# Kernel optimization log

Hardware: AMD Instinct MI355X
Metric: run time of the kernel (lower is better)

The kernel has to match this reference:

```python
import jax, jax.numpy as jnp
import numpy as np

BN_EPS = 1e-5

def _conv1x1(x, w, b):
    # x: [B,C,H,W], w: [O,C], b: [O] -> [B,O,H,W]
    return jnp.einsum('bchw,oc->bohw', x, w) + b[None, :, None, None]

def _maxpool2(x):
    B, C, H, W = x.shape
    return x.reshape(B, C, H // 2, 2, W // 2, 2).max(axis=(3, 5))

def setup_inputs() -> dict:
    key = jax.random.key(0)
    ks = jax.random.split(key, 5)
    B, C, Cint, H, W = 8, 512, 256, 64, 64
    s = 1.0 / np.sqrt(C)
    s2 = 1.0 / np.sqrt(Cint)
    return {
        'x': jax.random.normal(ks[0], (B, C, H, W), jnp.float32),
        'g_w': jax.random.normal(ks[1], (Cint, C), jnp.float32) * s,
        'g_b': jnp.zeros((Cint,), jnp.float32),
        'theta_w': jax.random.normal(ks[2], (Cint, C), jnp.float32) * s,
        'theta_b': jnp.zeros((Cint,), jnp.float32),
        'phi_w': jax.random.normal(ks[3], (Cint, C), jnp.float32) * s,
        'phi_b': jnp.zeros((Cint,), jnp.float32),
        'w_w': jax.random.normal(ks[4], (C, Cint), jnp.float32) * s2,
        'w_b': jnp.zeros((C,), jnp.float32),
        'bn_gamma': jnp.ones((C,), jnp.float32),
        'bn_beta': jnp.zeros((C,), jnp.float32),
        'bn_mean': jnp.zeros((C,), jnp.float32),
        'bn_var': jnp.ones((C,), jnp.float32),
    }

def reference(x, g_w, g_b, theta_w, theta_b, phi_w, phi_b, w_w, w_b,
              bn_gamma, bn_beta, bn_mean, bn_var):
    B, C, H, W = x.shape
    Cint = g_w.shape[0]
    # projections (1x1 convs); g and phi are sub-sampled by MaxPool2d(2)
    xg = _maxpool2(_conv1x1(x, g_w, g_b)).reshape(B, Cint, -1)      # [B,Cint,M]
    xphi = _maxpool2(_conv1x1(x, phi_w, phi_b)).reshape(B, Cint, -1)  # [B,Cint,M]
    xth = _conv1x1(x, theta_w, theta_b).reshape(B, Cint, -1)        # [B,Cint,N]
    # affinity: theta^T @ phi -> [B,N,M], softmax over M
    f = jax.nn.softmax(jnp.einsum('bcn,bcm->bnm', xth, xphi), axis=-1)
    # weighted sum: f @ g^T -> [B,N,Cint] -> [B,Cint,H,W]
    y = jnp.einsum('bnm,bcm->bcn', f, xg).reshape(B, Cint, H, W)
    # output conv + batchnorm (inference form) + residual
    z = _conv1x1(y, w_w, w_b)
    inv = jax.lax.rsqrt(bn_var + BN_EPS)
    z = (z - bn_mean[None, :, None, None]) * (bn_gamma * inv)[None, :, None, None] + bn_beta[None, :, None, None]
    return z + x
```

## Files before the change

kernel.cpp:

```cpp
#include <hip/hip_runtime.h>
#include <cmath>


#define B_  8
#define C_  512
#define CI_ 256
#define N_  4096
#define M_  1024

typedef _Float16 half8 __attribute__((ext_vector_type(8)));
typedef _Float16 half4 __attribute__((ext_vector_type(4)));
typedef float    f32x4 __attribute__((ext_vector_type(4)));

__global__ __launch_bounds__(256) void wconv_kernel(
    const float* __restrict__ g_w, const float* __restrict__ th_w,
    const float* __restrict__ ph_w, const float* __restrict__ w_w,
    _Float16* __restrict__ wAll, _Float16* __restrict__ w16)
{
    const int i = blockIdx.x * 256 + threadIdx.x;
    if (i < 768 * 512) {
        const int o = i >> 9, c = i & 511;
        const float v = (o < 256) ? g_w[o * 512 + c]
                      : (o < 512) ? th_w[(o - 256) * 512 + c]
                                  : ph_w[(o - 512) * 512 + c];
        wAll[i] = (_Float16)v;
    } else {
        const int j = i - 768 * 512;
        w16[j] = (_Float16)w_w[j];
    }
}

__global__ __launch_bounds__(256) void xt_kernel(
    const float* __restrict__ x, _Float16* __restrict__ xT)
{
    __shared__ float Ls[64][68];
    const int t = threadIdx.x;
    const int n0 = blockIdx.x * 64, c0 = blockIdx.y * 64, b = blockIdx.z;

    const int row = t >> 4, coln = (t & 15) * 4;
    #pragma unroll
    for (int p = 0; p < 4; ++p) {
        const int c = p * 16 + row;
        *(float4*)&Ls[c][coln] = *(const float4*)&x[((size_t)b * C_ + c0 + c) * N_ + n0 + coln];
    }
    __syncthreads();
    const int nr = t >> 2, cq = (t & 3) * 16;
    _Float16 hv[16];
    #pragma unroll
    for (int j = 0; j < 16; ++j) hv[j] = (_Float16)Ls[cq + j][nr];
    _Float16* dst = &xT[((size_t)b * N_ + n0 + nr) * C_ + c0 + cq];
    *(half8*)&dst[0] = *(half8*)&hv[0];
    *(half8*)&dst[8] = *(half8*)&hv[8];
}

__global__ __launch_bounds__(256) void proj_kernel(
    const _Float16* __restrict__ xT, const _Float16* __restrict__ wAll,
    const float* __restrict__ g_b, const float* __restrict__ th_b,
    const float* __restrict__ ph_b,
    _Float16* __restrict__ thT, _Float16* __restrict__ phT, _Float16* __restrict__ g16)
{
    __shared__ __align__(16) char smem[27648];
    _Float16 (*Ws)[72] = (_Float16(*)[72])smem;
    _Float16 (*Xs)[72] = (_Float16(*)[72])(smem + 9216);
    _Float16 (*Yt)[72] = (_Float16(*)[72])smem;
    _Float16 (*Pp)[72] = (_Float16(*)[72])smem;
    _Float16 (*Pg)[40] = (_Float16(*)[40])smem;

    const int t = threadIdx.x;
    const int w = t >> 6, l = t & 63, l15 = l & 15, lg = l >> 4;
    const int bx = blockIdx.x, rt = blockIdx.y, b = blockIdx.z;
    const int r0 = rt * 64, n0 = bx * 128;

    f32x4 acc[8];
    #pragma unroll
    for (int f = 0; f < 8; ++f) acc[f] = (f32x4){0.f, 0.f, 0.f, 0.f};

    const int warow = t >> 2, wakq = (t & 3) * 16;
    const int xrow = t >> 1,  xkq = (t & 1) * 32;

    #pragma unroll 1
    for (int k0 = 0; k0 < C_; k0 += 64) {
        __syncthreads();
        {
            const _Float16* src = &wAll[(size_t)(r0 + warow) * C_ + k0 + wakq];
            *(half8*)&Ws[warow][wakq]     = *(const half8*)&src[0];
            *(half8*)&Ws[warow][wakq + 8] = *(const half8*)&src[8];
            const _Float16* xs = &xT[((size_t)b * N_ + n0 + xrow) * C_ + k0 + xkq];
            *(half8*)&Xs[xrow][xkq]      = *(const half8*)&xs[0];
            *(half8*)&Xs[xrow][xkq + 8]  = *(const half8*)&xs[8];
            *(half8*)&Xs[xrow][xkq + 16] = *(const half8*)&xs[16];
            *(half8*)&Xs[xrow][xkq + 24] = *(const half8*)&xs[24];
        }
        __syncthreads();
        #pragma unroll
        for (int ks = 0; ks < 2; ++ks) {
            half8 a = *(half8*)&Ws[w * 16 + l15][ks * 32 + lg * 8];
            #pragma unroll
            for (int f = 0; f < 8; ++f) {
                half8 bb = *(half8*)&Xs[f * 16 + l15][ks * 32 + lg * 8];
                acc[f] = __builtin_amdgcn_mfma_f32_16x16x32_f16(a, bb, acc[f], 0, 0, 0);
            }
        }
    }

    {
        const float* Bp = (rt < 4) ? g_b : (rt < 8) ? th_b : ph_b;
        const int coff = (rt < 4) ? 0 : (rt < 8) ? 256 : 512;
        float bias[4];
        #pragma unroll
        for (int r = 0; r < 4; ++r) bias[r] = Bp[r0 - coff + w * 16 + lg * 4 + r];
        #pragma unroll
        for (int f = 0; f < 8; ++f)
            #pragma unroll
            for (int r = 0; r < 4; ++r) acc[f][r] += bias[r];
    }

    if (rt >= 4 && rt < 8) {
        const int c0 = r0 - 256;
        __syncthreads();
        #pragma unroll
        for (int f = 0; f < 8; ++f) {
            half4 hv = { (_Float16)acc[f][0], (_Float16)acc[f][1],
                         (_Float16)acc[f][2], (_Float16)acc[f][3] };
            *(half4*)&Yt[f * 16 + l15][w * 16 + lg * 4] = hv;
        }
        __syncthreads();
        const int nr = t >> 1, oq = (t & 1) * 32;
        _Float16* dst = &thT[((size_t)b * N_ + n0 + nr) * CI_ + c0 + oq];
        #pragma unroll
        for (int j = 0; j < 4; ++j)
            *(half8*)&dst[j * 8] = *(half8*)&Yt[nr][oq + j * 8];
    } else {
        float pool[4][4];
        #pragma unroll
        for (int f = 0; f < 4; ++f)
            #pragma unroll
            for (int r = 0; r < 4; ++r) {
                const float v0 = acc[f][r], v1 = acc[f + 4][r];
                const float h0 = fmaxf(v0, __shfl_xor(v0, 1));
                const float h1 = fmaxf(v1, __shfl_xor(v1, 1));
                pool[f][r] = fmaxf(h0, h1);
            }
        __syncthreads();
        const bool isphi = (rt >= 8);
        const int c0 = isphi ? r0 - 512 : r0;
        if ((l15 & 1) == 0) {
            const int Wl = l15 >> 1;
            if (isphi) {
                #pragma unroll
                for (int f = 0; f < 4; ++f) {
                    half4 hv = { (_Float16)pool[f][0], (_Float16)pool[f][1],
                                 (_Float16)pool[f][2], (_Float16)pool[f][3] };
                    *(half4*)&Pp[f * 8 + Wl][w * 16 + lg * 4] = hv;
                }
            } else {
                #pragma unroll
                for (int f = 0; f < 4; ++f)
                    #pragma unroll
                    for (int r = 0; r < 4; ++r)
                        Pg[w * 16 + lg * 4 + r][f * 8 + Wl] = (_Float16)pool[f][r];
            }
        }
        __syncthreads();
        if (isphi) {
            const int row = t >> 3, cqq = (t & 7) * 8;
            *(half8*)&phT[((size_t)b * M_ + bx * 32 + row) * CI_ + c0 + cqq] =
                *(half8*)&Pp[row][cqq];
        } else {
            const int row = t >> 2, mq = (t & 3) * 8;
            *(half8*)&g16[((size_t)b * CI_ + r0 + row) * M_ + bx * 32 + mq] =
                *(half8*)&Pg[row][mq];
        }
    }
}

__global__ __launch_bounds__(256) void attn_kernel(
    const _Float16* __restrict__ thT, const _Float16* __restrict__ phT,
    const _Float16* __restrict__ g16, _Float16* __restrict__ y16)
{
    __shared__ __align__(16) char smem[61440];
    _Float16 (*Tl)[264] = (_Float16(*)[264])smem;
    _Float16 (*Ph)[72]  = (_Float16(*)[72])(smem + 33792);
    _Float16 (*Gl)[72]  = (_Float16(*)[72])(smem + 43008);
    _Float16 (*Pl)[72]  = (_Float16(*)[72])(smem + 52224);
    float    (*Yb)[69]  = (float(*)[69])(smem + 33792);

    const int t = threadIdx.x;
    const int w = t >> 6, l = t & 63;
    const int l15 = l & 15, lg = l >> 4;
    const int n0 = blockIdx.x * 64;
    const int b  = blockIdx.y;

    {
        const int row = t >> 2, cq = (t & 3) * 64;
        const _Float16* src = &thT[((size_t)b * N_ + n0 + row) * CI_ + cq];
        #pragma unroll
        for (int i = 0; i < 8; ++i)
            *(half8*)&Tl[row][cq + 8 * i] = *(const half8*)&src[8 * i];
    }

    f32x4 yacc[16];
    #pragma unroll
    for (int i = 0; i < 16; ++i) yacc[i] = (f32x4){0.f, 0.f, 0.f, 0.f};
    float m_run[4] = {-INFINITY, -INFINITY, -INFINITY, -INFINITY};
    float l_run[4] = {0.f, 0.f, 0.f, 0.f};

    const int srow = t >> 2, ssq = (t & 3) * 16;

    #pragma unroll 1
    for (int mt = 0; mt < 16; ++mt) {
        const int m0 = mt * 64;
        f32x4 sf[4];
        #pragma unroll
        for (int i = 0; i < 4; ++i) sf[i] = (f32x4){0.f, 0.f, 0.f, 0.f};

        #pragma unroll 1
        for (int cch = 0; cch < 4; ++cch) {
            __syncthreads();
            const _Float16* src = &phT[((size_t)b * M_ + m0 + srow) * CI_ + cch * 64 + ssq];
            *(half8*)&Ph[srow][ssq]     = *(const half8*)&src[0];
            *(half8*)&Ph[srow][ssq + 8] = *(const half8*)&src[8];
            __syncthreads();
            #pragma unroll
            for (int ks = 0; ks < 2; ++ks) {
                half8 a = *(half8*)&Tl[w * 16 + l15][cch * 64 + ks * 32 + lg * 8];
                #pragma unroll
                for (int mf = 0; mf < 4; ++mf) {
                    half8 bb = *(half8*)&Ph[mf * 16 + l15][ks * 32 + lg * 8];
                    sf[mf] = __builtin_amdgcn_mfma_f32_16x16x32_f16(a, bb, sf[mf], 0, 0, 0);
                }
            }
        }

        float sc[4];
        #pragma unroll
        for (int r = 0; r < 4; ++r) {
            float mx = fmaxf(fmaxf(sf[0][r], sf[1][r]), fmaxf(sf[2][r], sf[3][r]));
            #pragma unroll
            for (int off = 1; off < 16; off <<= 1) mx = fmaxf(mx, __shfl_xor(mx, off, 64));
            const float mnew = fmaxf(m_run[r], mx);
            sc[r] = __expf(m_run[r] - mnew);
            float sum = 0.f;
            #pragma unroll
            for (int mf = 0; mf < 4; ++mf) {
                const float p = __expf(sf[mf][r] - mnew);
                Pl[w * 16 + lg * 4 + r][mf * 16 + l15] = (_Float16)p;
                sum += p;
            }
            #pragma unroll
            for (int off = 1; off < 16; off <<= 1) sum += __shfl_xor(sum, off, 64);
            l_run[r] = l_run[r] * sc[r] + sum;
            m_run[r] = mnew;
        }
        #pragma unroll
        for (int i = 0; i < 16; ++i) {
            yacc[i][0] *= sc[0]; yacc[i][1] *= sc[1];
            yacc[i][2] *= sc[2]; yacc[i][3] *= sc[3];
        }

        #pragma unroll
        for (int cc = 0; cc < 4; ++cc) {
            __syncthreads();
            const _Float16* gs = &g16[((size_t)b * CI_ + cc * 64 + srow) * M_ + m0 + ssq];
            *(half8*)&Gl[srow][ssq]     = *(const half8*)&gs[0];
            *(half8*)&Gl[srow][ssq + 8] = *(const half8*)&gs[8];
            __syncthreads();
            half8 pa0 = *(half8*)&Pl[w * 16 + l15][lg * 8];
            half8 pa1 = *(half8*)&Pl[w * 16 + l15][32 + lg * 8];
            #pragma unroll
            for (int cf = 0; cf < 4; ++cf) {
                half8 b0 = *(half8*)&Gl[cf * 16 + l15][lg * 8];
                half8 b1 = *(half8*)&Gl[cf * 16 + l15][32 + lg * 8];
                yacc[cc * 4 + cf] = __builtin_amdgcn_mfma_f32_16x16x32_f16(pa0, b0, yacc[cc * 4 + cf], 0, 0, 0);
                yacc[cc * 4 + cf] = __builtin_amdgcn_mfma_f32_16x16x32_f16(pa1, b1, yacc[cc * 4 + cf], 0, 0, 0);
            }
        }
    }

    float linv[4];
    #pragma unroll
    for (int r = 0; r < 4; ++r) linv[r] = 1.f / l_run[r];
    #pragma unroll
    for (int cq = 0; cq < 4; ++cq) {
        __syncthreads();
        #pragma unroll
        for (int f = 0; f < 4; ++f)
            #pragma unroll
            for (int r = 0; r < 4; ++r)
                Yb[w * 16 + lg * 4 + r][f * 16 + l15] = yacc[cq * 4 + f][r] * linv[r];
        __syncthreads();
        const int row = t >> 2, cil = (t & 3) * 16;
        _Float16 hv[16];
        #pragma unroll
        for (int j = 0; j < 16; ++j) hv[j] = (_Float16)Yb[row][cil + j];
        _Float16* dst = &y16[((size_t)b * N_ + n0 + row) * CI_ + cq * 64 + cil];
        *(half8*)&dst[0] = *(half8*)&hv[0];
        *(half8*)&dst[8] = *(half8*)&hv[8];
    }
}

__global__ __launch_bounds__(256) void out_kernel(
    const _Float16* __restrict__ y16, const _Float16* __restrict__ w16,
    const float* __restrict__ w_b,
    const float* __restrict__ bn_g, const float* __restrict__ bn_b,
    const float* __restrict__ bn_m, const float* __restrict__ bn_v,
    const float* __restrict__ x, float* __restrict__ out)
{
    __shared__ __align__(16) char smem[33792];
    _Float16 (*Ws)[72] = (_Float16(*)[72])smem;
    _Float16 (*Ys)[72] = (_Float16(*)[72])(smem + 9216);
    float    (*Yt)[132] = (float(*)[132])smem;

    const int t = threadIdx.x;
    const int w = t >> 6, l = t & 63, l15 = l & 15, lg = l >> 4;
    const int bx = blockIdx.x, by = blockIdx.y, b = blockIdx.z;
    const int r0 = by * 64, n0 = bx * 128;

    f32x4 acc[8];
    #pragma unroll
    for (int f = 0; f < 8; ++f) acc[f] = (f32x4){0.f, 0.f, 0.f, 0.f};

    const int warow = t >> 2, wakq = (t & 3) * 16;
    const int yrow = t >> 1,  ykq = (t & 1) * 32;

    #pragma unroll 1
    for (int k0 = 0; k0 < CI_; k0 += 64) {
        __syncthreads();
        {
            const _Float16* src = &w16[(size_t)(r0 + warow) * CI_ + k0 + wakq];
            *(half8*)&Ws[warow][wakq]     = *(const half8*)&src[0];
            *(half8*)&Ws[warow][wakq + 8] = *(const half8*)&src[8];
            const _Float16* ys = &y16[((size_t)b * N_ + n0 + yrow) * CI_ + k0 + ykq];
            *(half8*)&Ys[yrow][ykq]      = *(const half8*)&ys[0];
            *(half8*)&Ys[yrow][ykq + 8]  = *(const half8*)&ys[8];
            *(half8*)&Ys[yrow][ykq + 16] = *(const half8*)&ys[16];
            *(half8*)&Ys[yrow][ykq + 24] = *(const half8*)&ys[24];
        }
        __syncthreads();
        #pragma unroll
        for (int ks = 0; ks < 2; ++ks) {
            half8 a = *(half8*)&Ws[w * 16 + l15][ks * 32 + lg * 8];
            #pragma unroll
            for (int f = 0; f < 8; ++f) {
                half8 bb = *(half8*)&Ys[f * 16 + l15][ks * 32 + lg * 8];
                acc[f] = __builtin_amdgcn_mfma_f32_16x16x32_f16(a, bb, acc[f], 0, 0, 0);
            }
        }
    }

    float scp[4], shp[4];
    #pragma unroll
    for (int r = 0; r < 4; ++r) {
        const int c = r0 + w * 16 + lg * 4 + r;
        const float s = bn_g[c] * rsqrtf(bn_v[c] + 1e-5f);
        scp[r] = s;
        shp[r] = bn_b[c] + (w_b[c] - bn_m[c]) * s;
    }
    __syncthreads();
    #pragma unroll
    for (int f = 0; f < 8; ++f)
        #pragma unroll
        for (int r = 0; r < 4; ++r)
            Yt[w * 16 + lg * 4 + r][f * 16 + l15] = acc[f][r] * scp[r] + shp[r];
    __syncthreads();

    const int prow = t >> 5, nq = (t & 31) * 4;
    #pragma unroll
    for (int p = 0; p < 8; ++p) {
        const int row = p * 8 + prow;
        const size_t base = ((size_t)b * C_ + r0 + row) * N_ + n0 + nq;
        const float4 xr = *(const float4*)&x[base];
        float4 v = *(float4*)&Yt[row][nq];
        v.x += xr.x; v.y += xr.y; v.z += xr.z; v.w += xr.w;
        *(float4*)&out[base] = v;
    }
}

extern "C" void kernel_launch(void* const* d_in, const int* in_sizes, int n_in,
                              void* d_out, int out_size, void* d_ws, size_t ws_size,
                              hipStream_t stream) {
    const float* x    = (const float*)d_in[0];
    const float* g_w  = (const float*)d_in[1];
    const float* g_b  = (const float*)d_in[2];
    const float* th_w = (const float*)d_in[3];
    const float* th_b = (const float*)d_in[4];
    const float* ph_w = (const float*)d_in[5];
    const float* ph_b = (const float*)d_in[6];
    const float* w_w  = (const float*)d_in[7];
    const float* w_b  = (const float*)d_in[8];
    const float* bn_g = (const float*)d_in[9];
    const float* bn_b = (const float*)d_in[10];
    const float* bn_m = (const float*)d_in[11];
    const float* bn_v = (const float*)d_in[12];
    float* out = (float*)d_out;

    _Float16* xT   = (_Float16*)d_ws;
    _Float16* wAll = xT + (size_t)B_ * N_ * C_;
    _Float16* w16  = wAll + 768 * 512;
    _Float16* thT  = w16 + 512 * 256;
    _Float16* phT  = thT + (size_t)B_ * N_ * CI_;
    _Float16* g16  = phT + (size_t)B_ * M_ * CI_;
    _Float16* y16  = g16 + (size_t)B_ * M_ * CI_;

    wconv_kernel<<<2048, 256, 0, stream>>>(g_w, th_w, ph_w, w_w, wAll, w16);
    xt_kernel<<<dim3(64, 8, 8), 256, 0, stream>>>(x, xT);
    proj_kernel<<<dim3(32, 12, 8), 256, 0, stream>>>(xT, wAll, g_b, th_b, ph_b,
                                                     thT, phT, g16);
    attn_kernel<<<dim3(64, 8), 256, 0, stream>>>(thT, phT, g16, y16);
    out_kernel<<<dim3(32, 8, 8), 256, 0, stream>>>(y16, w16, w_b, bn_g, bn_b, bn_m, bn_v,
                                                   x, out);
}
```

Baseline: 339.5 us.

## Restructure attention kernel with transposed MFMA, register-resident theta and shuffle-built P

The attention kernel swaps MFMA operand roles so each lane owns one query row. Theta fragments stay in registers instead of LDS, the softmax row reductions shrink to two shuffles, and the P tile is rebuilt through lane shuffles rather than an LDS round-trip. Phi is staged once per tile (full 256 channels) and g in two 128-channel halves, which cuts the number of barriers. The output is written straight from registers, and the smaller LDS footprint plus launch bounds of 3 aim for higher occupancy, at the cost of register pressure from keeping theta in registers.

```diff
diff --git a/kernel.cpp b/kernel.cpp
--- a/kernel.cpp
+++ b/kernel.cpp
@@ -11,6 +11,13 @@
 typedef _Float16 half8 __attribute__((ext_vector_type(8)));
 typedef _Float16 half4 __attribute__((ext_vector_type(4)));
 typedef float    f32x4 __attribute__((ext_vector_type(4)));
+
+static __device__ __forceinline__ unsigned pkh(float a, float b) {
+    _Float16 ha = (_Float16)a, hb = (_Float16)b;
+    unsigned short ua = __builtin_bit_cast(unsigned short, ha);
+    unsigned short ub = __builtin_bit_cast(unsigned short, hb);
+    return (unsigned)ua | ((unsigned)ub << 16);
+}
 
 __global__ __launch_bounds__(256) void wconv_kernel(
     const float* __restrict__ g_w, const float* __restrict__ th_w,
@@ -174,128 +181,143 @@
     }
 }
 
-__global__ __launch_bounds__(256) void attn_kernel(
+__global__ __launch_bounds__(256, 3) void attn_kernel(
     const _Float16* __restrict__ thT, const _Float16* __restrict__ phT,
     const _Float16* __restrict__ g16, _Float16* __restrict__ y16)
 {
-    __shared__ __align__(16) char smem[61440];
-    _Float16 (*Tl)[264] = (_Float16(*)[264])smem;
-    _Float16 (*Ph)[72]  = (_Float16(*)[72])(smem + 33792);
-    _Float16 (*Gl)[72]  = (_Float16(*)[72])(smem + 43008);
-    _Float16 (*Pl)[72]  = (_Float16(*)[72])(smem + 52224);
-    float    (*Yb)[69]  = (float(*)[69])(smem + 33792);
+    __shared__ __align__(16) char smem[52224];
+    _Float16 (*Ph)[264] = (_Float16(*)[264])smem;
+    _Float16 (*Gl)[72]  = (_Float16(*)[72])(smem + 33792);
 
     const int t = threadIdx.x;
     const int w = t >> 6, l = t & 63;
     const int l15 = l & 15, lg = l >> 4;
     const int n0 = blockIdx.x * 64;
     const int b  = blockIdx.y;
-
+    const int n  = n0 + w * 16 + l15;
+
+    half8 ta[8];
     {
-        const int row = t >> 2, cq = (t & 3) * 64;
-        const _Float16* src = &thT[((size_t)b * N_ + n0 + row) * CI_ + cq];
-        #pragma unroll
-        for (int i = 0; i < 8; ++i)
-            *(half8*)&Tl[row][cq + 8 * i] = *(const half8*)&src[8 * i];
+        const _Float16* src = &thT[((size_t)b * N_ + n) * CI_ + lg * 8];
+        #pragma unroll
+        for (int kc = 0; kc < 8; ++kc)
+            ta[kc] = *(const half8*)&src[kc * 32];
     }
 
     f32x4 yacc[16];
     #pragma unroll
     for (int i = 0; i < 16; ++i) yacc[i] = (f32x4){0.f, 0.f, 0.f, 0.f};
-    float m_run[4] = {-INFINITY, -INFINITY, -INFINITY, -INFINITY};
-    float l_run[4] = {0.f, 0.f, 0.f, 0.f};
-
-    const int srow = t >> 2, ssq = (t & 3) * 16;
+    float m_run = -INFINITY, l_run = 0.f;
+
+    const int phrow = t >> 2, phseg = (t & 3) * 64;
+    const int glrow = t >> 1, glseg = (t & 1) * 32;
+
+    const int baseA = ((lg & 1) * 2) * 16 + l15;
+    const int baseB = baseA + 16;
+    const bool hi = ((lg >> 1) & 1) != 0;
 
     #pragma unroll 1
     for (int mt = 0; mt < 16; ++mt) {
         const int m0 = mt * 64;
+
+        __syncthreads();
+        {
+            const _Float16* src = &phT[((size_t)b * M_ + m0 + phrow) * CI_ + phseg];
+            #pragma unroll
+            for (int j = 0; j < 8; ++j)
+                *(half8*)&Ph[phrow][phseg + j * 8] = *(const half8*)&src[j * 8];
+        }
+        __syncthreads();
+
         f32x4 sf[4];
         #pragma unroll
         for (int i = 0; i < 4; ++i) sf[i] = (f32x4){0.f, 0.f, 0.f, 0.f};
-
-        #pragma unroll 1
-        for (int cch = 0; cch < 4; ++cch) {
+        #pragma unroll
+        for (int kc = 0; kc < 8; ++kc) {
+            #pragma unroll
+            for (int mf = 0; mf < 4; ++mf) {
+                half8 a = *(half8*)&Ph[mf * 16 + l15][kc * 32 + lg * 8];
+                sf[mf] = __builtin_amdgcn_mfma_f32_16x16x32_f16(a, ta[kc], sf[mf], 0, 0, 0);
+            }
+        }
+
+        float mx = sf[0][0];
+        #pragma unroll
+        for (int mf = 0; mf < 4; ++mf)
+            #pragma unroll
+            for (int r = 0; r < 4; ++r) mx = fmaxf(mx, sf[mf][r]);
+        mx = fmaxf(mx, __shfl_xor(mx, 16, 64));
+        mx = fmaxf(mx, __shfl_xor(mx, 32, 64));
+        const float mnew = fmaxf(m_run, mx);
+        const float scl = __expf(m_run - mnew);
+        float s = 0.f;
+        unsigned u0[4], u1[4];
+        #pragma unroll
+        for (int mf = 0; mf < 4; ++mf) {
+            const float p0 = __expf(sf[mf][0] - mnew);
+            const float p1 = __expf(sf[mf][1] - mnew);
+            const float p2 = __expf(sf[mf][2] - mnew);
+            const float p3 = __expf(sf[mf][3] - mnew);
+            s += (p0 + p1) + (p2 + p3);
+            u0[mf] = pkh(p0, p1);
+            u1[mf] = pkh(p2, p3);
+        }
+        s += __shfl_xor(s, 16, 64);
+        s += __shfl_xor(s, 32, 64);
+        l_run = l_run * scl + s;
+        m_run = mnew;
+        #pragma unroll
+        for (int i = 0; i < 16; ++i) {
+            yacc[i][0] *= scl; yacc[i][1] *= scl;
+            yacc[i][2] *= scl; yacc[i][3] *= scl;
+        }
+
+        half8 pb[2];
+        #pragma unroll
+        for (int ks = 0; ks < 2; ++ks) {
+            const unsigned a0 = __shfl(u0[2 * ks],     baseA, 64);
+            const unsigned a1 = __shfl(u1[2 * ks],     baseA, 64);
+            const unsigned c0 = __shfl(u0[2 * ks + 1], baseA, 64);
+            const unsigned c1 = __shfl(u1[2 * ks + 1], baseA, 64);
+            const unsigned b0 = __shfl(u0[2 * ks],     baseB, 64);
+            const unsigned b1 = __shfl(u1[2 * ks],     baseB, 64);
+            const unsigned d0 = __shfl(u0[2 * ks + 1], baseB, 64);
+            const unsigned d1 = __shfl(u1[2 * ks + 1], baseB, 64);
+            union { unsigned u[4]; half8 h; } cv;
+            cv.u[0] = hi ? c0 : a0;
+            cv.u[1] = hi ? c1 : a1;
+            cv.u[2] = hi ? d0 : b0;
+            cv.u[3] = hi ? d1 : b1;
+            pb[ks] = cv.h;
+        }
+
+        #pragma unroll
+        for (int ch = 0; ch < 2; ++ch) {
             __syncthreads();
-            const _Float16* src = &phT[((size_t)b * M_ + m0 + srow) * CI_ + cch * 64 + ssq];
-            *(half8*)&Ph[srow][ssq]     = *(const half8*)&src[0];
-            *(half8*)&Ph[srow][ssq + 8] = *(const half8*)&src[8];
+            {
+                const _Float16* src = &g16[((size_t)b * CI_ + ch * 128 + glrow) * M_ + m0 + glseg];
+                #pragma unroll
+                for (int j = 0; j < 4; ++j)
+                    *(half8*)&Gl[glrow][glseg + j * 8] = *(const half8*)&src[j * 8];
+            }
             __syncthreads();
             #pragma unroll
-            for (int ks = 0; ks < 2; ++ks) {
-                half8 a = *(half8*)&Tl[w * 16 + l15][cch * 64 + ks * 32 + lg * 8];
-                #pragma unroll
-                for (int mf = 0; mf < 4; ++mf) {
-                    half8 bb = *(half8*)&Ph[mf * 16 + l15][ks * 32 + lg * 8];
-                    sf[mf] = __builtin_amdgcn_mfma_f32_16x16x32_f16(a, bb, sf[mf], 0, 0, 0);
-                }
-            }
-        }
-
-        float sc[4];
-        #pragma unroll
-        for (int r = 0; r < 4; ++r) {
-            float mx = fmaxf(fmaxf(sf[0][r], sf[1][r]), fmaxf(sf[2][r], sf[3][r]));
-            #pragma unroll
-            for (int off = 1; off < 16; off <<= 1) mx = fmaxf(mx, __shfl_xor(mx, off, 64));
-            const float mnew = fmaxf(m_run[r], mx);
-            sc[r] = __expf(m_run[r] - mnew);
-            float sum = 0.f;
-            #pragma unroll
-            for (int mf = 0; mf < 4; ++mf) {
-                const float p = __expf(sf[mf][r] - mnew);
-                Pl[w * 16 + lg * 4 + r][mf * 16 + l15] = (_Float16)p;
-                sum += p;
-            }
-            #pragma unroll
-            for (int off = 1; off < 16; off <<= 1) sum += __shfl_xor(sum, off, 64);
-            l_run[r] = l_run[r] * sc[r] + sum;
-            m_run[r] = mnew;
-        }
-        #pragma unroll
-        for (int i = 0; i < 16; ++i) {
-            yacc[i][0] *= sc[0]; yacc[i][1] *= sc[1];
-            yacc[i][2] *= sc[2]; yacc[i][3] *= sc[3];
-        }
-
-        #pragma unroll
-        for (int cc = 0; cc < 4; ++cc) {
-            __syncthreads();
-            const _Float16* gs = &g16[((size_t)b * CI_ + cc * 64 + srow) * M_ + m0 + ssq];
-            *(half8*)&Gl[srow][ssq]     = *(const half8*)&gs[0];
-            *(half8*)&Gl[srow][ssq + 8] = *(const half8*)&gs[8];
-            __syncthreads();
-            half8 pa0 = *(half8*)&Pl[w * 16 + l15][lg * 8];
-            half8 pa1 = *(half8*)&Pl[w * 16 + l15][32 + lg * 8];
-            #pragma unroll
-            for (int cf = 0; cf < 4; ++cf) {
-                half8 b0 = *(half8*)&Gl[cf * 16 + l15][lg * 8];
-                half8 b1 = *(half8*)&Gl[cf * 16 + l15][32 + lg * 8];
-                yacc[cc * 4 + cf] = __builtin_amdgcn_mfma_f32_16x16x32_f16(pa0, b0, yacc[cc * 4 + cf], 0, 0, 0);
-                yacc[cc * 4 + cf] = __builtin_amdgcn_mfma_f32_16x16x32_f16(pa1, b1, yacc[cc * 4 + cf], 0, 0, 0);
-            }
-        }
-    }
-
-    float linv[4];
-    #pragma unroll
-    for (int r = 0; r < 4; ++r) linv[r] = 1.f / l_run[r];
-    #pragma unroll
-    for (int cq = 0; cq < 4; ++cq) {
-        __syncthreads();
-        #pragma unroll
-        for (int f = 0; f < 4; ++f)
-            #pragma unroll
-            for (int r = 0; r < 4; ++r)
-                Yb[w * 16 + lg * 4 + r][f * 16 + l15] = yacc[cq * 4 + f][r] * linv[r];
-        __syncthreads();
-        const int row = t >> 2, cil = (t & 3) * 16;
-        _Float16 hv[16];
-        #pragma unroll
-        for (int j = 0; j < 16; ++j) hv[j] = (_Float16)Yb[row][cil + j];
-        _Float16* dst = &y16[((size_t)b * N_ + n0 + row) * CI_ + cq * 64 + cil];
-        *(half8*)&dst[0] = *(half8*)&hv[0];
-        *(half8*)&dst[8] = *(half8*)&hv[8];
+            for (int cf = 0; cf < 8; ++cf) {
+                half8 a0 = *(half8*)&Gl[cf * 16 + l15][lg * 8];
+                half8 a1 = *(half8*)&Gl[cf * 16 + l15][32 + lg * 8];
+                yacc[ch * 8 + cf] = __builtin_amdgcn_mfma_f32_16x16x32_f16(a0, pb[0], yacc[ch * 8 + cf], 0, 0, 0);
+                yacc[ch * 8 + cf] = __builtin_amdgcn_mfma_f32_16x16x32_f16(a1, pb[1], yacc[ch * 8 + cf], 0, 0, 0);
+            }
+        }
+    }
+
+    const float linv = 1.f / l_run;
+    _Float16* dst = &y16[((size_t)b * N_ + n) * CI_];
+    #pragma unroll
+    for (int q = 0; q < 16; ++q) {
+        half4 hv = { (_Float16)(yacc[q][0] * linv), (_Float16)(yacc[q][1] * linv),
+                     (_Float16)(yacc[q][2] * linv), (_Float16)(yacc[q][3] * linv) };
+        *(half4*)&dst[q * 16 + lg * 4] = hv;
     }
 }
 
```

Result: slower. 348.4 us (+2.6%).
